# Kernel tuning notes

Hardware: AMD Instinct MI355X
Metric: run time of the kernel (lower is better)

The kernel has to match this reference:

```python
import jax, jax.numpy as jnp
import numpy as np

N_HEADS = 16


def setup_inputs() -> dict:
    key = jax.random.key(0)
    ks = jax.random.split(key, 9)
    B, S, D = 2, 2048, 2048
    s = 0.02
    return {
        "X": jax.random.normal(ks[0], (B, S, D), jnp.float32),
        "Wq": jax.random.normal(ks[1], (D, D), jnp.float32) * s,
        "bq": jax.random.normal(ks[2], (D,), jnp.float32) * s,
        "Wk": jax.random.normal(ks[3], (D, D), jnp.float32) * s,
        "bk": jax.random.normal(ks[4], (D,), jnp.float32) * s,
        "Wv": jax.random.normal(ks[5], (D, D), jnp.float32) * s,
        "bv": jax.random.normal(ks[6], (D,), jnp.float32) * s,
        "Wo": jax.random.normal(ks[7], (D, D), jnp.float32) * s,
        "bo": jax.random.normal(ks[8], (D,), jnp.float32) * s,
    }


def reference(X, Wq, bq, Wk, bk, Wv, bv, Wo, bo):
    B, S, D = X.shape
    H = N_HEADS
    d_head = D // H
    # qk_scale = 1/sqrt(sqrt(d_head)), applied to BOTH Q and K
    scale = jnp.asarray(1.0 / np.sqrt(np.sqrt(d_head)), X.dtype)
    Q = (X @ Wq.T + bq).reshape(B, S, H, d_head) * scale  # bqhd
    K = (X @ Wk.T + bk).reshape(B, S, H, d_head) * scale  # bkhd
    V = (X @ Wv.T + bv).reshape(B, S, H, d_head)          # bkhd
    scores = jnp.einsum("bqhd,bkhd->bhqk", Q, K)
    causal = jnp.tril(jnp.ones((S, S), bool))  # [q, k]
    scores = jnp.where(causal[None, None], scores, -jnp.inf)
    # original casts logits to fp32 before softmax, back to Q dtype after
    attn = jax.nn.softmax(scores.astype(jnp.float32), axis=-1).astype(X.dtype)
    out = jnp.einsum("bhqk,bkhd->bqhd", attn, V).reshape(B, S, D)
    return out @ Wo.T + bo
```

## Files before the change

### kernel.cpp

```cpp
#include <hip/hip_runtime.h>


typedef __attribute__((ext_vector_type(8))) short bfx8;
typedef __attribute__((ext_vector_type(4))) float f32x4;

#define TO_GLOBAL(p) ((const __attribute__((address_space(1))) void*)(p))
#define TO_LDS(p)    ((__attribute__((address_space(3))) void*)(p))

__device__ __forceinline__ unsigned short f2bf(float f) {
    unsigned int u = __float_as_uint(f);
    u += 0x7FFFu + ((u >> 16) & 1u);
    return (unsigned short)(u >> 16);
}

__device__ __forceinline__ void store_out(unsigned short* p, float v) { *p = f2bf(v); }
__device__ __forceinline__ void store_out(float* p, float v) { *p = v; }

__global__ void cast_bf16_kernel(const float* __restrict__ x,
                                 unsigned short* __restrict__ y, int n4) {
    int i = blockIdx.x * blockDim.x + threadIdx.x;
    int st = gridDim.x * blockDim.x;
    for (; i < n4; i += st) {
        float4 v = reinterpret_cast<const float4*>(x)[i];
        ushort4 o;
        o.x = f2bf(v.x); o.y = f2bf(v.y); o.z = f2bf(v.z); o.w = f2bf(v.w);
        reinterpret_cast<ushort4*>(y)[i] = o;
    }
}

__global__ void cast3_kernel(const float* __restrict__ s0, const float* __restrict__ s1,
                             const float* __restrict__ s2,
                             unsigned short* __restrict__ d0, unsigned short* __restrict__ d1,
                             unsigned short* __restrict__ d2, int n4) {
    const float* s = (blockIdx.y == 0) ? s0 : (blockIdx.y == 1) ? s1 : s2;
    unsigned short* d = (blockIdx.y == 0) ? d0 : (blockIdx.y == 1) ? d1 : d2;
    int i = blockIdx.x * blockDim.x + threadIdx.x;
    int st = gridDim.x * blockDim.x;
    for (; i < n4; i += st) {
        float4 v = reinterpret_cast<const float4*>(s)[i];
        ushort4 o;
        o.x = f2bf(v.x); o.y = f2bf(v.y); o.z = f2bf(v.z); o.w = f2bf(v.w);
        reinterpret_cast<ushort4*>(d)[i] = o;
    }
}

template <typename OUT>
__global__ __launch_bounds__(256) void gemm_bt(
    const unsigned short* __restrict__ A, const unsigned short* __restrict__ Bw,
    const float* __restrict__ bias, OUT* __restrict__ C,
    int M, int N, int K, float scale) {
    __shared__ __align__(16) unsigned short Ash[128 * 32];
    __shared__ __align__(16) unsigned short Bsh[128 * 32];

    const int tid  = threadIdx.x;
    const int lane = tid & 63;
    const int w    = tid >> 6;
    const int g    = lane >> 4;
    const int l15  = lane & 15;
    const int m0   = blockIdx.y * 128;
    const int n0   = blockIdx.x * 128;
    const int wm   = (w >> 1) * 64;
    const int wn   = (w & 1) * 64;

    f32x4 acc[4][4];
#pragma unroll
    for (int i = 0; i < 4; i++)
#pragma unroll
        for (int j = 0; j < 4; j++) acc[i][j] = (f32x4){0.f, 0.f, 0.f, 0.f};

    const int c0 = tid, c1 = tid + 256;
    const int rowA0 = c0 >> 2, colA0 = (c0 & 3) * 8;
    const int rowA1 = c1 >> 2, colA1 = (c1 & 3) * 8;

    for (int k0 = 0; k0 < K; k0 += 32) {
        __syncthreads();
        __builtin_amdgcn_global_load_lds(TO_GLOBAL(A + (size_t)(m0 + rowA0) * K + k0 + colA0),
                                         TO_LDS(&Ash[c0 * 8]), 16, 0, 0);
        __builtin_amdgcn_global_load_lds(TO_GLOBAL(A + (size_t)(m0 + rowA1) * K + k0 + colA1),
                                         TO_LDS(&Ash[c1 * 8]), 16, 0, 0);
        __builtin_amdgcn_global_load_lds(TO_GLOBAL(Bw + (size_t)(n0 + rowA0) * K + k0 + colA0),
                                         TO_LDS(&Bsh[c0 * 8]), 16, 0, 0);
        __builtin_amdgcn_global_load_lds(TO_GLOBAL(Bw + (size_t)(n0 + rowA1) * K + k0 + colA1),
                                         TO_LDS(&Bsh[c1 * 8]), 16, 0, 0);
        __syncthreads();

        bfx8 af[4], bfr[4];
#pragma unroll
        for (int mi = 0; mi < 4; mi++)
            af[mi] = *reinterpret_cast<const bfx8*>(&Ash[(wm + mi * 16 + l15) * 32 + g * 8]);
#pragma unroll
        for (int ni = 0; ni < 4; ni++)
            bfr[ni] = *reinterpret_cast<const bfx8*>(&Bsh[(wn + ni * 16 + l15) * 32 + g * 8]);
#pragma unroll
        for (int mi = 0; mi < 4; mi++)
#pragma unroll
            for (int ni = 0; ni < 4; ni++)
                acc[mi][ni] = __builtin_amdgcn_mfma_f32_16x16x32_bf16(af[mi], bfr[ni],
                                                                     acc[mi][ni], 0, 0, 0);
    }

#pragma unroll
    for (int mi = 0; mi < 4; mi++) {
#pragma unroll
        for (int ni = 0; ni < 4; ni++) {
            const int col = n0 + wn + ni * 16 + l15;
            const float bv = bias[col];
#pragma unroll
            for (int r = 0; r < 4; r++) {
                const int row = m0 + wm + mi * 16 + g * 4 + r;
                store_out(&C[(size_t)row * N + col], (acc[mi][ni][r] + bv) * scale);
            }
        }
    }
}

__global__ __launch_bounds__(512, 2) void gemm256_qkv(
    const unsigned short* __restrict__ A,
    const unsigned short* __restrict__ W0, const unsigned short* __restrict__ W1,
    const unsigned short* __restrict__ W2,
    const float* __restrict__ b0p, const float* __restrict__ b1p,
    const float* __restrict__ b2p,
    unsigned short* __restrict__ C0, unsigned short* __restrict__ C1,
    unsigned short* __restrict__ C2, float qks) {
    __shared__ __align__(16) unsigned short Ash[32768];
    __shared__ __align__(16) unsigned short Bsh[32768];

    const int z = blockIdx.z;
    const unsigned short* Bw = (z == 0) ? W0 : (z == 1) ? W1 : W2;
    const float* bias = (z == 0) ? b0p : (z == 1) ? b1p : b2p;
    unsigned short* C = (z == 0) ? C0 : (z == 1) ? C1 : C2;
    const float scale = (z < 2) ? qks : 1.0f;

    const int tid  = threadIdx.x;
    const int lane = tid & 63;
    const int w    = tid >> 6;
    const int g    = lane >> 4;
    const int l15  = lane & 15;
    const int wm   = w >> 2;
    const int wn   = w & 3;
    const int m0   = blockIdx.y * 256;
    const int n0   = blockIdx.x * 256;
    const int sch  = tid & 7;

    f32x4 acc[8][4];
#pragma unroll
    for (int i = 0; i < 8; i++)
#pragma unroll
        for (int j = 0; j < 4; j++) acc[i][j] = (f32x4){0.f, 0.f, 0.f, 0.f};

#define STG_A(BUF, H, KB)                                                            \
    do {                                                                             \
        _Pragma("unroll")                                                            \
        for (int L_ = 0; L_ < 2; ++L_) {                                             \
            const int r_ = L_ * 64 + (tid >> 3);                                     \
            __builtin_amdgcn_global_load_lds(                                        \
                TO_GLOBAL(A + (size_t)(m0 + (H) * 128 + r_) * 2048 + (KB) +          \
                          ((sch ^ (r_ & 7)) * 8)),                                   \
                TO_LDS(Ash + (BUF) * 16384 + (H) * 8192 + L_ * 4096 + tid * 8),      \
                16, 0, 0);                                                           \
        }                                                                            \
    } while (0)
#define STG_B(BUF, H, KB)                                                            \
    do {                                                                             \
        _Pragma("unroll")                                                            \
        for (int L_ = 0; L_ < 2; ++L_) {                                             \
            const int r_ = L_ * 64 + (tid >> 3);                                     \
            __builtin_amdgcn_global_load_lds(                                        \
                TO_GLOBAL(Bw + (size_t)(n0 + (H) * 128 + r_) * 2048 + (KB) +         \
                          ((sch ^ (r_ & 7)) * 8)),                                   \
                TO_LDS(Bsh + (BUF) * 16384 + (H) * 8192 + L_ * 4096 + tid * 8),      \
                16, 0, 0);                                                           \
        }                                                                            \
    } while (0)

#define RD_A(DST, BUF, MH)                                                           \
    _Pragma("unroll")                                                                \
    for (int mi = 0; mi < 4; mi++)                                                   \
        _Pragma("unroll")                                                            \
        for (int kc = 0; kc < 2; kc++) {                                             \
            const int r_ = (MH) * 64 + mi * 16 + l15;                                \
            DST[mi][kc] = *(const bfx8*)(Ash + (BUF) * 16384 + wm * 8192 +           \
                                         r_ * 64 + (((kc * 4 + g) ^ (r_ & 7)) * 8)); \
        }
#define RD_B(DST, BUF, NH)                                                           \
    _Pragma("unroll")                                                                \
    for (int ni = 0; ni < 2; ni++)                                                   \
        _Pragma("unroll")                                                            \
        for (int kc = 0; kc < 2; kc++) {                                             \
            const int r_ = (wn & 1) * 64 + (NH) * 32 + ni * 16 + l15;                \
            DST[ni][kc] = *(const bfx8*)(Bsh + (BUF) * 16384 + (wn >> 1) * 8192 +    \
                                         r_ * 64 + (((kc * 4 + g) ^ (r_ & 7)) * 8)); \
        }
#define MFMA16(AF, BF, MH, NH)                                                       \
    __builtin_amdgcn_s_setprio(1);                                                   \
    _Pragma("unroll")                                                                \
    for (int kc = 0; kc < 2; kc++)                                                   \
        _Pragma("unroll")                                                            \
        for (int mi = 0; mi < 4; mi++)                                               \
            _Pragma("unroll")                                                        \
            for (int ni = 0; ni < 2; ni++)                                           \
                acc[(MH) * 4 + mi][(NH) * 2 + ni] =                                  \
                    __builtin_amdgcn_mfma_f32_16x16x32_bf16(                         \
                        AF[mi][kc], BF[ni][kc], acc[(MH) * 4 + mi][(NH) * 2 + ni],   \
                        0, 0, 0);                                                    \
    __builtin_amdgcn_s_setprio(0);

    STG_A(0, 0, 0); STG_A(0, 1, 0); STG_B(0, 0, 0); STG_B(0, 1, 0);

    bfx8 a0[4][2], a1[4][2], bb[2][2];

#pragma unroll 1
    for (int t = 0; t < 32; ++t) {
        const int kb  = t * 64;
        const int buf = t & 1;
        const bool pf = (t + 1 < 32);

        if (pf) {
            STG_A(buf ^ 1, 0, kb + 64);
            asm volatile("s_waitcnt vmcnt(2)" ::: "memory");
        } else {
            asm volatile("s_waitcnt vmcnt(0)" ::: "memory");
        }
        RD_A(a0, buf, 0);
        RD_B(bb, buf, 0);
        __builtin_amdgcn_s_barrier();
        asm volatile("s_waitcnt lgkmcnt(0)" ::: "memory");
        __builtin_amdgcn_sched_barrier(0);
        MFMA16(a0, bb, 0, 0);
        __builtin_amdgcn_s_barrier();

        if (pf) STG_A(buf ^ 1, 1, kb + 64);
        RD_B(bb, buf, 1);
        __builtin_amdgcn_s_barrier();
        asm volatile("s_waitcnt lgkmcnt(0)" ::: "memory");
        __builtin_amdgcn_sched_barrier(0);
        MFMA16(a0, bb, 0, 1);
        __builtin_amdgcn_s_barrier();

        if (pf) STG_B(buf ^ 1, 0, kb + 64);
        RD_A(a1, buf, 1);
        __builtin_amdgcn_s_barrier();
        asm volatile("s_waitcnt lgkmcnt(0)" ::: "memory");
        __builtin_amdgcn_sched_barrier(0);
        MFMA16(a1, bb, 1, 1);
        __builtin_amdgcn_s_barrier();

        if (pf) STG_B(buf ^ 1, 1, kb + 64);
        RD_B(bb, buf, 0);
        __builtin_amdgcn_s_barrier();
        asm volatile("s_waitcnt lgkmcnt(0)" ::: "memory");
        __builtin_amdgcn_sched_barrier(0);
        MFMA16(a1, bb, 1, 0);
        __builtin_amdgcn_s_barrier();
    }

#pragma unroll
    for (int mf = 0; mf < 8; mf++) {
#pragma unroll
        for (int nf = 0; nf < 4; nf++) {
            const int col = n0 + wn * 64 + nf * 16 + l15;
            const float bv = bias[col];
#pragma unroll
            for (int r = 0; r < 4; r++) {
                const int row = m0 + wm * 128 + mf * 16 + g * 4 + r;
                C[(size_t)row * 2048 + col] = f2bf((acc[mf][nf][r] + bv) * scale);
            }
        }
    }
#undef STG_A
#undef STG_B
#undef RD_A
#undef RD_B
#undef MFMA16
}

__global__ __launch_bounds__(256) void transpose_v(const unsigned short* __restrict__ V,
                                                   unsigned short* __restrict__ Vt) {
    __shared__ unsigned short tile[64][72];
    const int tid = threadIdx.x;
    const int r0 = blockIdx.y * 64;
    const int c0 = blockIdx.x * 64;
    const int b = r0 >> 11, sbase = r0 & 2047;
#pragma unroll
    for (int i = 0; i < 2; i++) {
        const int row = tid >> 2;
        const int ch  = (tid & 3) + 4 * i;
        bfx8 v = *reinterpret_cast<const bfx8*>(V + (size_t)(r0 + row) * 2048 + c0 + ch * 8);
        *reinterpret_cast<bfx8*>(&tile[row][ch * 8]) = v;
    }
    __syncthreads();
    const int dh  = tid & 63;
    const int s_l = (tid >> 6) * 16;
    unsigned short* dst = Vt + (size_t)(b * 2048 + c0 + dh) * 2048 + sbase + s_l;
#pragma unroll
    for (int half = 0; half < 2; half++) {
        bfx8 o;
#pragma unroll
        for (int j = 0; j < 8; j++) o[j] = (short)tile[s_l + half * 8 + j][dh];
        *reinterpret_cast<bfx8*>(dst + half * 8) = o;
    }
}

#define SLEN 2048
#define DMODEL 2048
#define M2FIX 11.541560327f

__global__ __launch_bounds__(256, 3) void attn_kernel(
    const unsigned short* __restrict__ Q, const unsigned short* __restrict__ Kp,
    const unsigned short* __restrict__ Vt, unsigned short* __restrict__ O) {
    __shared__ __align__(16) unsigned short Ksh[64 * 128];
    __shared__ __align__(16) unsigned short Vsh[128 * 64];
    __shared__ __align__(16) unsigned short Psh[4 * 1024];

    const int tid  = threadIdx.x;
    const int lane = tid & 63;
    const int w    = tid >> 6;
    const int g    = lane >> 4;
    const int l15  = lane & 15;
    const int bh   = blockIdx.x;
    const int b    = bh >> 4, h = bh & 15;
    const int pr   = blockIdx.y;

    const size_t bhbase = (size_t)b * SLEN * DMODEL + (size_t)h * 128;
    const size_t vtbase = (size_t)bh * 128 * SLEN;

    unsigned short* Pw = &Psh[w * 1024];
    const int khi_b = l15 >> 3, klo = l15 & 7;
    const int vsw = l15 & 7;

    const int krow = tid >> 4, kch = tid & 15;
    const int vdr  = tid >> 3, vch = tid & 7;

    bfx8 kreg[4], vreg[4];

#define LOADREGS(KB)                                                                \
    {                                                                               \
        _Pragma("unroll")                                                           \
        for (int i_ = 0; i_ < 4; i_++)                                              \
            kreg[i_] = *reinterpret_cast<const bfx8*>(                              \
                Kp + bhbase + (size_t)((KB) + krow + 16 * i_) * DMODEL + kch * 8);  \
        _Pragma("unroll")                                                           \
        for (int i_ = 0; i_ < 4; i_++)                                              \
            vreg[i_] = *reinterpret_cast<const bfx8*>(                              \
                Vt + vtbase + (size_t)(vdr + 32 * i_) * SLEN + (KB) + vch * 8);     \
    }

#pragma unroll 1
    for (int seg = 0; seg < 2; seg++) {
        const int qt  = seg == 0 ? (31 - pr) : pr;
        const int q0w = qt * 64 + w * 16;

        bfx8 qf[4];
#pragma unroll
        for (int c = 0; c < 4; c++)
            qf[c] = *reinterpret_cast<const bfx8*>(
                Q + bhbase + (size_t)(q0w + l15) * DMODEL + c * 32 + g * 8);

        f32x4 oacc[8];
#pragma unroll
        for (int i = 0; i < 8; i++) oacc[i] = (f32x4){0.f, 0.f, 0.f, 0.f};
        float lpart[4] = {0.f, 0.f, 0.f, 0.f};

        const int ntile = qt + 1;
        LOADREGS(0);

#pragma unroll 1
        for (int t = 0; t < ntile; t++) {
            const int kb = t * 64;
            __builtin_amdgcn_s_barrier();
            __builtin_amdgcn_sched_barrier(0);
#pragma unroll
            for (int i = 0; i < 4; i++) {
                const int row = krow + 16 * i;
                *reinterpret_cast<bfx8*>(&Ksh[row * 128 + ((kch ^ (row & 7)) * 8)]) = kreg[i];
            }
#pragma unroll
            for (int i = 0; i < 4; i++) {
                const int dr = vdr + 32 * i;
                *reinterpret_cast<bfx8*>(&Vsh[dr * 64 + ((vch ^ (dr & 7)) * 8)]) = vreg[i];
            }
            asm volatile("s_waitcnt lgkmcnt(0)" ::: "memory");
            __builtin_amdgcn_s_barrier();
            __builtin_amdgcn_sched_barrier(0);
            if (t + 1 < ntile) LOADREGS(kb + 64);

            __builtin_amdgcn_s_setprio(1);
            f32x4 sacc[4];
#pragma unroll
            for (int kt = 0; kt < 4; kt++) sacc[kt] = (f32x4){0.f, 0.f, 0.f, 0.f};
#pragma unroll
            for (int kt = 0; kt < 4; kt++) {
                const int row = kt * 16 + l15;
#pragma unroll
                for (int c = 0; c < 4; c++) {
                    bfx8 kf = *reinterpret_cast<const bfx8*>(
                        &Ksh[row * 128 + (((c * 4 + g) ^ (row & 7)) * 8)]);
                    sacc[kt] = __builtin_amdgcn_mfma_f32_16x16x32_bf16(
                        qf[c], kf, sacc[kt], 0, 0, 0);
                }
            }
            __builtin_amdgcn_s_setprio(0);
            if (t == ntile - 1) {
#pragma unroll
                for (int kt = 0; kt < 4; kt++)
#pragma unroll
                    for (int r = 0; r < 4; r++)
                        if (kb + kt * 16 + l15 > q0w + g * 4 + r)
                            sacc[kt][r] = -1e30f;
            }
#pragma unroll
            for (int r = 0; r < 4; r++) {
                const float p0 = exp2f(sacc[0][r] - M2FIX);
                const float p1 = exp2f(sacc[1][r] - M2FIX);
                const float p2 = exp2f(sacc[2][r] - M2FIX);
                const float p3 = exp2f(sacc[3][r] - M2FIX);
                lpart[r] += (p0 + p1) + (p2 + p3);
                const int ql = g * 4 + r;
                const int swz = ql & 7;
                Pw[ql * 64 + (((khi_b + 0) ^ swz) << 3) + klo] = f2bf(p0);
                Pw[ql * 64 + (((khi_b + 2) ^ swz) << 3) + klo] = f2bf(p1);
                Pw[ql * 64 + (((khi_b + 4) ^ swz) << 3) + klo] = f2bf(p2);
                Pw[ql * 64 + (((khi_b + 6) ^ swz) << 3) + klo] = f2bf(p3);
            }
            __builtin_amdgcn_s_setprio(1);
#pragma unroll
            for (int ks = 0; ks < 2; ks++) {
                bfx8 vb[8];
#pragma unroll
                for (int ni = 0; ni < 8; ni++) {
                    const int d = ni * 16 + l15;
                    vb[ni] = *reinterpret_cast<const bfx8*>(
                        &Vsh[d * 64 + (((ks * 4 + g) ^ vsw) * 8)]);
                }
                bfx8 pa = *reinterpret_cast<const bfx8*>(
                    Pw + l15 * 64 + (((ks * 4 + g) ^ vsw) << 3));
#pragma unroll
                for (int ni = 0; ni < 8; ni++)
                    oacc[ni] = __builtin_amdgcn_mfma_f32_16x16x32_bf16(
                        pa, vb[ni], oacc[ni], 0, 0, 0);
            }
            __builtin_amdgcn_s_setprio(0);
        }

#pragma unroll
        for (int r = 0; r < 4; r++) {
            float l = lpart[r];
#pragma unroll
            for (int s = 1; s < 16; s <<= 1) l += __shfl_xor(l, s);
            const float inv = 1.0f / l;
            const int q = q0w + g * 4 + r;
#pragma unroll
            for (int ni = 0; ni < 8; ni++)
                O[bhbase + (size_t)q * DMODEL + ni * 16 + l15] = f2bf(oacc[ni][r] * inv);
        }
    }
#undef LOADREGS
}

extern "C" void kernel_launch(void* const* d_in, const int* in_sizes, int n_in,
                              void* d_out, int out_size, void* d_ws, size_t ws_size,
                              hipStream_t stream) {
    const float* X  = (const float*)d_in[0];
    const float* Wq = (const float*)d_in[1];
    const float* bq = (const float*)d_in[2];
    const float* Wk = (const float*)d_in[3];
    const float* bk = (const float*)d_in[4];
    const float* Wv = (const float*)d_in[5];
    const float* bv = (const float*)d_in[6];
    const float* Wo = (const float*)d_in[7];
    const float* bo = (const float*)d_in[8];
    float* out = (float*)d_out;

    unsigned short* ws  = (unsigned short*)d_ws;
    unsigned short* Qb  = ws;
    unsigned short* Kb  = ws + 8388608;
    unsigned short* Vtb = ws + 16777216;
    unsigned short* XOb = ws + 25165824;
    unsigned short* Wb  = ws + 33554432;
    unsigned short* out_u   = (unsigned short*)d_out;
    unsigned short* Vstage  = out_u;
    unsigned short* Wkb     = out_u + 8388608;
    unsigned short* Wvb     = out_u + 12582912;

    const float qk_scale = 0.35709585f;

    const dim3 cb(256);

    cast_bf16_kernel<<<dim3(2048), cb, 0, stream>>>(X, XOb, 2097152);
    cast3_kernel<<<dim3(1024, 3), cb, 0, stream>>>(Wq, Wk, Wv, Wb, Wkb, Wvb, 1048576);

    gemm256_qkv<<<dim3(8, 16, 3), dim3(512), 0, stream>>>(XOb, Wb, Wkb, Wvb, bq, bk, bv,
                                                          Qb, Kb, Vstage, qk_scale);

    transpose_v<<<dim3(32, 64), cb, 0, stream>>>(Vstage, Vtb);

    attn_kernel<<<dim3(32, 16), cb, 0, stream>>>(Qb, Kb, Vtb, XOb);

    cast_bf16_kernel<<<dim3(1024), cb, 0, stream>>>(Wo, Wb, 1048576);
    gemm_bt<float><<<dim3(16, 32), cb, 0, stream>>>(XOb, Wb, bo, out, 4096, 2048, 2048, 1.0f);
}
```

Measured before the change: 347.0 us.

## Fuse V transpose into QKV GEMM epilogue and loosen vmcnt waits

```diff
diff --git a/kernel.cpp b/kernel.cpp
--- a/kernel.cpp
+++ b/kernel.cpp
@@ -217,7 +217,7 @@
 
         if (pf) {
             STG_A(buf ^ 1, 0, kb + 64);
-            asm volatile("s_waitcnt vmcnt(2)" ::: "memory");
+            asm volatile("s_waitcnt vmcnt(4)" ::: "memory");
         } else {
             asm volatile("s_waitcnt vmcnt(0)" ::: "memory");
         }
@@ -229,7 +229,10 @@
         MFMA16(a0, bb, 0, 0);
         __builtin_amdgcn_s_barrier();
 
-        if (pf) STG_A(buf ^ 1, 1, kb + 64);
+        if (pf) {
+            STG_A(buf ^ 1, 1, kb + 64);
+            asm volatile("s_waitcnt vmcnt(4)" ::: "memory");
+        }
         RD_B(bb, buf, 1);
         __builtin_amdgcn_s_barrier();
         asm volatile("s_waitcnt lgkmcnt(0)" ::: "memory");
@@ -254,16 +257,36 @@
         __builtin_amdgcn_s_barrier();
     }
 
-#pragma unroll
-    for (int mf = 0; mf < 8; mf++) {
-#pragma unroll
-        for (int nf = 0; nf < 4; nf++) {
-            const int col = n0 + wn * 64 + nf * 16 + l15;
-            const float bv = bias[col];
-#pragma unroll
-            for (int r = 0; r < 4; r++) {
-                const int row = m0 + wm * 128 + mf * 16 + g * 4 + r;
-                C[(size_t)row * 2048 + col] = f2bf((acc[mf][nf][r] + bv) * scale);
+    if (z == 2) {
+        const int b_ = m0 >> 11;
+        const int sbase = (m0 & 2047) + wm * 128;
+#pragma unroll
+        for (int mf = 0; mf < 8; mf++) {
+#pragma unroll
+            for (int nf = 0; nf < 4; nf++) {
+                const int col = n0 + wn * 64 + nf * 16 + l15;
+                const float bv = bias[col];
+                const int s0 = sbase + mf * 16 + g * 4;
+                ushort4 o;
+                o.x = f2bf(acc[mf][nf][0] + bv);
+                o.y = f2bf(acc[mf][nf][1] + bv);
+                o.z = f2bf(acc[mf][nf][2] + bv);
+                o.w = f2bf(acc[mf][nf][3] + bv);
+                *reinterpret_cast<ushort4*>(C + ((size_t)(b_ * 2048 + col)) * 2048 + s0) = o;
+            }
+        }
+    } else {
+#pragma unroll
+        for (int mf = 0; mf < 8; mf++) {
+#pragma unroll
+            for (int nf = 0; nf < 4; nf++) {
+                const int col = n0 + wn * 64 + nf * 16 + l15;
+                const float bv = bias[col];
+#pragma unroll
+                for (int r = 0; r < 4; r++) {
+                    const int row = m0 + wm * 128 + mf * 16 + g * 4 + r;
+                    C[(size_t)row * 2048 + col] = f2bf((acc[mf][nf][r] + bv) * scale);
+                }
             }
         }
     }
@@ -272,33 +295,6 @@
 #undef RD_A
 #undef RD_B
 #undef MFMA16
-}
-
-__global__ __launch_bounds__(256) void transpose_v(const unsigned short* __restrict__ V,
-                                                   unsigned short* __restrict__ Vt) {
-    __shared__ unsigned short tile[64][72];
-    const int tid = threadIdx.x;
-    const int r0 = blockIdx.y * 64;
-    const int c0 = blockIdx.x * 64;
-    const int b = r0 >> 11, sbase = r0 & 2047;
-#pragma unroll
-    for (int i = 0; i < 2; i++) {
-        const int row = tid >> 2;
-        const int ch  = (tid & 3) + 4 * i;
-        bfx8 v = *reinterpret_cast<const bfx8*>(V + (size_t)(r0 + row) * 2048 + c0 + ch * 8);
-        *reinterpret_cast<bfx8*>(&tile[row][ch * 8]) = v;
-    }
-    __syncthreads();
-    const int dh  = tid & 63;
-    const int s_l = (tid >> 6) * 16;
-    unsigned short* dst = Vt + (size_t)(b * 2048 + c0 + dh) * 2048 + sbase + s_l;
-#pragma unroll
-    for (int half = 0; half < 2; half++) {
-        bfx8 o;
-#pragma unroll
-        for (int j = 0; j < 8; j++) o[j] = (short)tile[s_l + half * 8 + j][dh];
-        *reinterpret_cast<bfx8*>(dst + half * 8) = o;
-    }
 }
 
 #define SLEN 2048
@@ -477,10 +473,9 @@
     unsigned short* Vtb = ws + 16777216;
     unsigned short* XOb = ws + 25165824;
     unsigned short* Wb  = ws + 33554432;
-    unsigned short* out_u   = (unsigned short*)d_out;
-    unsigned short* Vstage  = out_u;
-    unsigned short* Wkb     = out_u + 8388608;
-    unsigned short* Wvb     = out_u + 12582912;
+    unsigned short* out_u = (unsigned short*)d_out;
+    unsigned short* Wkb   = out_u;
+    unsigned short* Wvb   = out_u + 4194304;
 
     const float qk_scale = 0.35709585f;
 
@@ -490,9 +485,7 @@
     cast3_kernel<<<dim3(1024, 3), cb, 0, stream>>>(Wq, Wk, Wv, Wb, Wkb, Wvb, 1048576);
 
     gemm256_qkv<<<dim3(8, 16, 3), dim3(512), 0, stream>>>(XOb, Wb, Wkb, Wvb, bq, bk, bv,
-                                                          Qb, Kb, Vstage, qk_scale);
-
-    transpose_v<<<dim3(32, 64), cb, 0, stream>>>(Vstage, Vtb);
+                                                          Qb, Kb, Vtb, qk_scale);
 
     attn_kernel<<<dim3(32, 16), cb, 0, stream>>>(Qb, Kb, Vtb, XOb);
 
```

Result: faster. 338.9 us (-2.4%).
